# Kernel optimization log

Hardware: AMD Instinct MI355X
Metric: run time of the kernel (lower is better)

Reference implementation:

```python
import jax, jax.numpy as jnp
import numpy as np

_DIMS = [15, 30, 60, 90, 120, 90, 60, 30, 15, 10, 5, 1]


def setup_inputs() -> dict:
    key = jax.random.key(0)
    keys = jax.random.split(key, 1 + 2 * 11)
    inp = {"x": jax.random.normal(keys[0], (524288, 15), dtype=jnp.float32)}
    for i in range(11):
        fan_in, fan_out = _DIMS[i], _DIMS[i + 1]
        bound = 1.0 / np.sqrt(fan_in)
        inp[f"W{i+1}"] = jax.random.uniform(keys[1 + 2 * i], (fan_out, fan_in), minval=-bound, maxval=bound, dtype=jnp.float32)
        inp[f"b{i+1}"] = jax.random.uniform(keys[2 + 2 * i], (fan_out,), minval=-bound, maxval=bound, dtype=jnp.float32)
    return inp


def reference(x, W1, b1, W2, b2, W3, b3, W4, b4, W5, b5, W6, b6, W7, b7, W8, b8, W9, b9, W10, b10, W11, b11):
    Ws = [W1, W2, W3, W4, W5, W6, W7, W8, W9, W10, W11]
    bs = [b1, b2, b3, b4, b5, b6, b7, b8, b9, b10, b11]
    h = x
    # 10 Linear+ReLU layers, funnel 15->30->60->90->120->90->60->30->15->10->5
    for W, b in zip(Ws[:-1], bs[:-1]):
        h = jax.nn.relu(h @ W.T + b)
    # final Linear 5->1 + sigmoid
    return jax.nn.sigmoid(h @ Ws[-1].T + bs[-1])
```

## Files before the change

### kernel.cpp

```cpp
#include <hip/hip_runtime.h>
#include <math.h>


using bf16x8 = __attribute__((ext_vector_type(8))) short;
using f32x4  = __attribute__((ext_vector_type(4))) float;
using u16x8  = __attribute__((ext_vector_type(8))) unsigned short;
using u32x2  = __attribute__((ext_vector_type(2))) unsigned;
using u32x4  = __attribute__((ext_vector_type(4))) unsigned;
typedef __bf16 bf16x2_t __attribute__((ext_vector_type(2)));

namespace {
constexpr int NL = 11;
constexpr int IN_[NL]   = {15, 30, 60, 90, 120, 90, 60, 30, 15, 10, 5};
constexpr int OUT_[NL]  = {30, 60, 90, 120, 90, 60, 30, 15, 10, 5, 1};
constexpr int KP_[NL]   = {32, 32, 64, 96, 128, 96, 64, 32, 32, 32, 32};
constexpr int NP_[NL]   = {32, 64, 96, 128, 96, 64, 32, 16, 16, 16, 16};
constexpr int WOFF_[NL] = {0, 1024, 3072, 9216, 21504, 33792, 39936, 41984, 42496, 43008, 43520};
constexpr int WTOT      = 44032;
constexpr int WAVES     = 8;
constexpr int ROWS_PER_BLOCK = 512;
constexpr int ARENA     = 4096;
constexpr int LDS_BYTES = (WTOT + WAVES * ARENA) * 2;
}

__device__ __forceinline__ unsigned short f2bf(float f) {
    unsigned u = __float_as_uint(f);
    u += 0x7fffu + ((u >> 16) & 1u);
    return (unsigned short)(u >> 16);
}

__device__ __forceinline__ unsigned pk2(float a, float b) {
#if __has_builtin(__builtin_amdgcn_cvt_pk_bf16_f32)
    return __builtin_bit_cast(unsigned, __builtin_amdgcn_cvt_pk_bf16_f32(a, b));
#else
    bf16x2_t c;
    c[0] = (__bf16)a;
    c[1] = (__bf16)b;
    return __builtin_bit_cast(unsigned, c);
#endif
}

__device__ __forceinline__ u32x2 packrelu(f32x4 a) {
    u32x2 p;
    p[0] = pk2(fmaxf(a[0], 0.f), fmaxf(a[1], 0.f));
    p[1] = pk2(fmaxf(a[2], 0.f), fmaxf(a[3], 0.f));
    return p;
}

__device__ __forceinline__ bf16x8 xform(u32x2 pa, u32x2 pb, bool sel, int sA, int sB) {
    int a0 = __shfl((int)pa[0], sA);
    int b0 = __shfl((int)pb[0], sA);
    int a1 = __shfl((int)pa[1], sA);
    int b1 = __shfl((int)pb[1], sA);
    int a2 = __shfl((int)pa[0], sB);
    int b2 = __shfl((int)pb[0], sB);
    int a3 = __shfl((int)pa[1], sB);
    int b3 = __shfl((int)pb[1], sB);
    u32x4 r;
    r[0] = (unsigned)(sel ? b0 : a0);
    r[1] = (unsigned)(sel ? b1 : a1);
    r[2] = (unsigned)(sel ? b2 : a2);
    r[3] = (unsigned)(sel ? b3 : a3);
    return __builtin_bit_cast(bf16x8, r);
}

template <int L>
__device__ __forceinline__ void stage_w(const float* __restrict__ W,
                                        const float* __restrict__ B,
                                        short* wlds, int tid) {
    constexpr int KP = KP_[L], NP = NP_[L], INl = IN_[L], OUTl = OUT_[L];
    constexpr int NKT = KP / 32;
    for (int idx = tid; idx < NP * KP; idx += 512) {
        const int f    = idx >> 9;
        const int t    = idx & 511;
        const int quad = t >> 7;
        const int colc = (t >> 3) & 15;
        const int j    = t & 7;
        const int mt   = f / NKT;
        const int kt   = f - mt * NKT;
        const int m    = mt * 16 + colc;
        const int k    = kt * 32 + quad * 8 + j;
        float v = 0.f;
        if (m < OUTl) {
            if (k < INl) v = W[m * INl + k];
            else if (k == INl) v = B[m];
            else if (k == INl + 1) {
                float hf = __builtin_bit_cast(float, (unsigned)f2bf(B[m]) << 16);
                v = B[m] - hf;
            }
        } else if (m == OUTl || m == OUTl + 1) {
            if (k == INl) v = 1.f;
        }
        wlds[WOFF_[L] + idx] = (short)f2bf(v);
    }
}

template <int L>
__device__ __forceinline__ void layer_lds(const short* __restrict__ wlds,
                                          short* buf, int col, int quad, int fo) {
    constexpr int NKT  = KP_[L] / 32;
    constexpr int NMT  = NP_[L] / 16;
    constexpr int NKTN = KP_[L + 1] / 32;
    const short* wl = wlds + WOFF_[L];
    bf16x8 bin[4][NKT];
#pragma unroll
    for (int t = 0; t < 4; ++t)
#pragma unroll
        for (int kt = 0; kt < NKT; ++kt)
            bin[t][kt] = *(const bf16x8*)(buf + (t * NKT + kt) * 512 + fo);
    f32x4 acc[NMT][4];
#pragma unroll
    for (int mt = 0; mt < NMT; ++mt)
#pragma unroll
        for (int t = 0; t < 4; ++t)
            acc[mt][t] = f32x4{0.f, 0.f, 0.f, 0.f};
#pragma unroll
    for (int kt = 0; kt < NKT; ++kt)
#pragma unroll
        for (int mt = 0; mt < NMT; ++mt) {
            bf16x8 af = *(const bf16x8*)(wl + (mt * NKT + kt) * 512 + fo);
#pragma unroll
            for (int t = 0; t < 4; ++t)
                acc[mt][t] = __builtin_amdgcn_mfma_f32_16x16x32_bf16(af, bin[t][kt], acc[mt][t], 0, 0, 0);
        }
#pragma unroll
    for (int mt = 0; mt < NMT; ++mt) {
        const int wbase = (mt >> 1) * 512 + ((mt & 1) * 2 + (quad >> 1)) * 128 + col * 8 + (quad & 1) * 4;
#pragma unroll
        for (int t = 0; t < 4; ++t)
            *(u32x2*)(buf + t * NKTN * 512 + wbase) = packrelu(acc[mt][t]);
    }
}

template <int L>
__device__ __forceinline__ void reg_pair(const short* __restrict__ wlds, int g,
                                         const bf16x8 (&bin)[KP_[L] / 32][4],
                                         bf16x8 (&bout)[4],
                                         bool sel, int sA, int sB, int fo) {
    constexpr int NKT = KP_[L] / 32;
    const short* wl = wlds + WOFF_[L];
    f32x4 acc0[4], acc1[4];
#pragma unroll
    for (int t = 0; t < 4; ++t) {
        acc0[t] = f32x4{0.f, 0.f, 0.f, 0.f};
        acc1[t] = f32x4{0.f, 0.f, 0.f, 0.f};
    }
#pragma unroll
    for (int kt = 0; kt < NKT; ++kt) {
        bf16x8 a0 = *(const bf16x8*)(wl + ((2 * g) * NKT + kt) * 512 + fo);
        bf16x8 a1 = *(const bf16x8*)(wl + ((2 * g + 1) * NKT + kt) * 512 + fo);
#pragma unroll
        for (int t = 0; t < 4; ++t) {
            acc0[t] = __builtin_amdgcn_mfma_f32_16x16x32_bf16(a0, bin[kt][t], acc0[t], 0, 0, 0);
            acc1[t] = __builtin_amdgcn_mfma_f32_16x16x32_bf16(a1, bin[kt][t], acc1[t], 0, 0, 0);
        }
    }
#pragma unroll
    for (int t = 0; t < 4; ++t)
        bout[t] = xform(packrelu(acc0[t]), packrelu(acc1[t]), sel, sA, sB);
}

__device__ __forceinline__ void l5_to_lds(const short* __restrict__ wlds,
                                          const bf16x8 (&h5)[3][4],
                                          short* buf, int col, int quad, int fo) {
    const short* wl = wlds + WOFF_[5];
    f32x4 acc[4][4];
#pragma unroll
    for (int mt = 0; mt < 4; ++mt)
#pragma unroll
        for (int t = 0; t < 4; ++t)
            acc[mt][t] = f32x4{0.f, 0.f, 0.f, 0.f};
#pragma unroll
    for (int kt = 0; kt < 3; ++kt)
#pragma unroll
        for (int mt = 0; mt < 4; ++mt) {
            bf16x8 af = *(const bf16x8*)(wl + (mt * 3 + kt) * 512 + fo);
#pragma unroll
            for (int t = 0; t < 4; ++t)
                acc[mt][t] = __builtin_amdgcn_mfma_f32_16x16x32_bf16(af, h5[kt][t], acc[mt][t], 0, 0, 0);
        }
#pragma unroll
    for (int mt = 0; mt < 4; ++mt) {
        const int wbase = (mt >> 1) * 512 + ((mt & 1) * 2 + (quad >> 1)) * 128 + col * 8 + (quad & 1) * 4;
#pragma unroll
        for (int t = 0; t < 4; ++t)
            *(u32x2*)(buf + t * 2 * 512 + wbase) = packrelu(acc[mt][t]);
    }
}

__device__ __forceinline__ void layer_one4(bf16x8 af, short* buf, int col, int quad, int fo) {
    bf16x8 b[4];
#pragma unroll
    for (int t = 0; t < 4; ++t) b[t] = *(const bf16x8*)(buf + t * 512 + fo);
    f32x4 a[4];
#pragma unroll
    for (int t = 0; t < 4; ++t) {
        a[t] = f32x4{0.f, 0.f, 0.f, 0.f};
        a[t] = __builtin_amdgcn_mfma_f32_16x16x32_bf16(af, b[t], a[t], 0, 0, 0);
    }
    const int wbase = (quad >> 1) * 128 + col * 8 + (quad & 1) * 4;
#pragma unroll
    for (int t = 0; t < 4; ++t)
        *(u32x2*)(buf + t * 512 + wbase) = packrelu(a[t]);
    u16x8 z = {0, 0, 0, 0, 0, 0, 0, 0};
    if (!(quad & 1)) z[0] = (unsigned short)0x3F80;
    *(u16x8*)(buf + (quad >> 1) * 512 + (2 + (quad & 1)) * 128 + col * 8) = z;
    *(u16x8*)(buf + ((quad >> 1) + 2) * 512 + (2 + (quad & 1)) * 128 + col * 8) = z;
}

__device__ __forceinline__ float4 ld4(const float* p) {
    float4 t;
    __builtin_memcpy(&t, p, 16);
    return t;
}

__device__ __forceinline__ void fetch_x4(const float* __restrict__ x, int row0,
                                         int col, int quad, float4 (&xv)[4]) {
#pragma unroll
    for (int t = 0; t < 4; ++t) {
        const float* xr = x + (long)(row0 + t * 16 + col) * 15;
        if (quad < 3) {
            xv[t] = ld4(xr + quad * 4);
        } else {
            float4 u = ld4(xr + 11);
            xv[t] = make_float4(u.y, u.z, u.w, 1.f);
        }
    }
}

__device__ __forceinline__ void stage_x4(short* buf, const float4 (&xv)[4],
                                         int col, int quad) {
    const int off = (quad >> 1) * 128 + col * 8 + (quad & 1) * 4;
#pragma unroll
    for (int t = 0; t < 4; ++t) {
        u32x2 o;
        o[0] = pk2(xv[t].x, xv[t].y);
        o[1] = pk2(xv[t].z, xv[t].w);
        *(u32x2*)(buf + t * 512 + off) = o;
    }
    u16x8 z = {0, 0, 0, 0, 0, 0, 0, 0};
    if (!(quad & 1)) z[0] = (unsigned short)0x3F80;
    *(u16x8*)(buf + (quad >> 1) * 512 + (2 + (quad & 1)) * 128 + col * 8) = z;
    *(u16x8*)(buf + ((quad >> 1) + 2) * 512 + (2 + (quad & 1)) * 128 + col * 8) = z;
}

extern "C" __global__ void __launch_bounds__(512, 2)
mlp_fused(const float* __restrict__ x,
          const float* __restrict__ W0,  const float* __restrict__ B0,
          const float* __restrict__ W1,  const float* __restrict__ B1,
          const float* __restrict__ W2,  const float* __restrict__ B2,
          const float* __restrict__ W3,  const float* __restrict__ B3,
          const float* __restrict__ W4,  const float* __restrict__ B4,
          const float* __restrict__ W5,  const float* __restrict__ B5,
          const float* __restrict__ W6,  const float* __restrict__ B6,
          const float* __restrict__ W7,  const float* __restrict__ B7,
          const float* __restrict__ W8,  const float* __restrict__ B8,
          const float* __restrict__ W9,  const float* __restrict__ B9,
          const float* __restrict__ W10, const float* __restrict__ B10,
          float* __restrict__ out, int nchunks) {
    extern __shared__ __align__(16) short smem[];
    short* wlds = smem;
    short* act  = smem + WTOT;

    const int tid = threadIdx.x;

    stage_w<0>(W0, B0, wlds, tid);
    stage_w<1>(W1, B1, wlds, tid);
    stage_w<2>(W2, B2, wlds, tid);
    stage_w<3>(W3, B3, wlds, tid);
    stage_w<4>(W4, B4, wlds, tid);
    stage_w<5>(W5, B5, wlds, tid);
    stage_w<6>(W6, B6, wlds, tid);
    stage_w<7>(W7, B7, wlds, tid);
    stage_w<8>(W8, B8, wlds, tid);
    stage_w<9>(W9, B9, wlds, tid);
    stage_w<10>(W10, B10, wlds, tid);
    __syncthreads();

    const int wave = tid >> 6;
    const int lane = tid & 63;
    const int col  = lane & 15;
    const int quad = lane >> 4;
    short* buf = act + wave * ARENA;
    const int fo = quad * 128 + col * 8;
    const bool sel = quad >= 2;
    const int sA = col + 16 * (2 * (quad & 1));
    const int sB = sA + 16;

    const bf16x8 w7  = *(const bf16x8*)(wlds + WOFF_[7]  + fo);
    const bf16x8 w8  = *(const bf16x8*)(wlds + WOFF_[8]  + fo);
    const bf16x8 w9  = *(const bf16x8*)(wlds + WOFF_[9]  + fo);
    const bf16x8 w10 = *(const bf16x8*)(wlds + WOFF_[10] + fo);

    int chunk = blockIdx.x;
    float4 xv[4];
    if (chunk < nchunks)
        fetch_x4(x, chunk * ROWS_PER_BLOCK + wave * 64, col, quad, xv);

    for (; chunk < nchunks; chunk += gridDim.x) {
        const int row0 = chunk * ROWS_PER_BLOCK + wave * 64;
        stage_x4(buf, xv, col, quad);

        const int nxt = chunk + gridDim.x;
        if (nxt < nchunks)
            fetch_x4(x, nxt * ROWS_PER_BLOCK + wave * 64, col, quad, xv);

        layer_lds<0>(wlds, buf, col, quad, fo);
        layer_lds<1>(wlds, buf, col, quad, fo);

        bf16x8 h2[2][4];
#pragma unroll
        for (int kt = 0; kt < 2; ++kt)
#pragma unroll
            for (int t = 0; t < 4; ++t)
                h2[kt][t] = *(const bf16x8*)(buf + (t * 2 + kt) * 512 + fo);

        bf16x8 h3[3][4];
#pragma unroll
        for (int g = 0; g < 3; ++g)
            reg_pair<2>(wlds, g, h2, h3[g], sel, sA, sB, fo);

        bf16x8 h4[4][4];
#pragma unroll
        for (int g = 0; g < 4; ++g)
            reg_pair<3>(wlds, g, h3, h4[g], sel, sA, sB, fo);

        bf16x8 h5[3][4];
#pragma unroll
        for (int g = 0; g < 3; ++g)
            reg_pair<4>(wlds, g, h4, h5[g], sel, sA, sB, fo);

        l5_to_lds(wlds, h5, buf, col, quad, fo);

        layer_lds<6>(wlds, buf, col, quad, fo);
        layer_one4(w7, buf, col, quad, fo);
        layer_one4(w8, buf, col, quad, fo);
        layer_one4(w9, buf, col, quad, fo);

        {
            f32x4 a[4];
#pragma unroll
            for (int t = 0; t < 4; ++t) {
                bf16x8 b = *(const bf16x8*)(buf + t * 512 + fo);
                a[t] = f32x4{0.f, 0.f, 0.f, 0.f};
                a[t] = __builtin_amdgcn_mfma_f32_16x16x32_bf16(w10, b, a[t], 0, 0, 0);
            }
            if (quad == 0) {
#pragma unroll
                for (int t = 0; t < 4; ++t)
                    out[row0 + t * 16 + col] = 1.f / (1.f + __expf(-a[t][0]));
            }
        }
    }
}

extern "C" void kernel_launch(void* const* d_in, const int* in_sizes, int n_in,
                              void* d_out, int out_size, void* d_ws, size_t ws_size,
                              hipStream_t stream) {
    (void)n_in; (void)d_ws; (void)ws_size; (void)out_size;
    const float* x = (const float*)d_in[0];
    const float* W[11];
    const float* B[11];
    for (int i = 0; i < 11; ++i) {
        W[i] = (const float*)d_in[1 + 2 * i];
        B[i] = (const float*)d_in[2 + 2 * i];
    }
    const int nrows   = in_sizes[0] / 15;
    const int nchunks = nrows / ROWS_PER_BLOCK;

    hipFuncSetAttribute((const void*)mlp_fused,
                        hipFuncAttributeMaxDynamicSharedMemorySize, LDS_BYTES);

    mlp_fused<<<dim3(256), dim3(512), LDS_BYTES, stream>>>(
        x,
        W[0], B[0], W[1], B[1], W[2], B[2], W[3], B[3], W[4], B[4],
        W[5], B[5], W[6], B[6], W[7], B[7], W[8], B[8], W[9], B[9],
        W[10], B[10],
        (float*)d_out, nchunks);
}
```

Measured before the change: 201.9 us.

## Pipeline MLP layers across waves with register-resident weights and LDS handoff

Result: slower. 212.6 us (+5.3%).

```diff
diff --git a/kernel.cpp b/kernel.cpp
--- a/kernel.cpp
+++ b/kernel.cpp
@@ -11,16 +11,19 @@
 
 namespace {
 constexpr int NL = 11;
-constexpr int IN_[NL]   = {15, 30, 60, 90, 120, 90, 60, 30, 15, 10, 5};
-constexpr int OUT_[NL]  = {30, 60, 90, 120, 90, 60, 30, 15, 10, 5, 1};
-constexpr int KP_[NL]   = {32, 32, 64, 96, 128, 96, 64, 32, 32, 32, 32};
-constexpr int NP_[NL]   = {32, 64, 96, 128, 96, 64, 32, 16, 16, 16, 16};
-constexpr int WOFF_[NL] = {0, 1024, 3072, 9216, 21504, 33792, 39936, 41984, 42496, 43008, 43520};
-constexpr int WTOT      = 44032;
-constexpr int WAVES     = 8;
-constexpr int ROWS_PER_BLOCK = 512;
-constexpr int ARENA     = 4096;
-constexpr int LDS_BYTES = (WTOT + WAVES * ARENA) * 2;
+constexpr int IN_[NL]  = {15, 30, 60, 90, 120, 90, 60, 30, 15, 10, 5};
+constexpr int OUT_[NL] = {30, 60, 90, 120, 90, 60, 30, 15, 10, 5, 1};
+constexpr int KP_[NL]  = {32, 32, 64, 96, 128, 96, 64, 32, 32, 32, 32};
+constexpr int NP_[NL]  = {32, 64, 96, 128, 96, 64, 32, 16, 16, 16, 16};
+constexpr int E0 = 0;
+constexpr int E1 = 1024;
+constexpr int E2 = 5120;
+constexpr int E3 = 11264;
+constexpr int E4 = 19456;
+constexpr int E5 = 25600;
+constexpr int LDS_SHORTS = 29696;
+constexpr int LDS_BYTES  = LDS_SHORTS * 2;
+constexpr int G = 32;
 }
 
 __device__ __forceinline__ unsigned short f2bf(float f) {
@@ -64,10 +67,26 @@
     return __builtin_bit_cast(bf16x8, r);
 }
 
+__device__ __forceinline__ bf16x8 xform16(u32x2 p, int quad, int sA16, int sB16) {
+    int d0 = __shfl((int)p[0], sA16);
+    int d1 = __shfl((int)p[1], sA16);
+    int d2 = __shfl((int)p[0], sB16);
+    int d3 = __shfl((int)p[1], sB16);
+    u32x4 r;
+    if (quad < 2) {
+        r[0] = (unsigned)d0; r[1] = (unsigned)d1;
+        r[2] = (unsigned)d2; r[3] = (unsigned)d3;
+    } else {
+        r[0] = (quad == 2) ? 0x00003F80u : 0u;
+        r[1] = 0u; r[2] = 0u; r[3] = 0u;
+    }
+    return __builtin_bit_cast(bf16x8, r);
+}
+
 template <int L>
 __device__ __forceinline__ void stage_w(const float* __restrict__ W,
                                         const float* __restrict__ B,
-                                        short* wlds, int tid) {
+                                        short* s, int tid) {
     constexpr int KP = KP_[L], NP = NP_[L], INl = IN_[L], OUTl = OUT_[L];
     constexpr int NKT = KP / 32;
     for (int idx = tid; idx < NP * KP; idx += 512) {
@@ -91,121 +110,15 @@
         } else if (m == OUTl || m == OUTl + 1) {
             if (k == INl) v = 1.f;
         }
-        wlds[WOFF_[L] + idx] = (short)f2bf(v);
-    }
-}
-
-template <int L>
-__device__ __forceinline__ void layer_lds(const short* __restrict__ wlds,
-                                          short* buf, int col, int quad, int fo) {
-    constexpr int NKT  = KP_[L] / 32;
-    constexpr int NMT  = NP_[L] / 16;
-    constexpr int NKTN = KP_[L + 1] / 32;
-    const short* wl = wlds + WOFF_[L];
-    bf16x8 bin[4][NKT];
-#pragma unroll
-    for (int t = 0; t < 4; ++t)
-#pragma unroll
-        for (int kt = 0; kt < NKT; ++kt)
-            bin[t][kt] = *(const bf16x8*)(buf + (t * NKT + kt) * 512 + fo);
-    f32x4 acc[NMT][4];
-#pragma unroll
-    for (int mt = 0; mt < NMT; ++mt)
-#pragma unroll
-        for (int t = 0; t < 4; ++t)
-            acc[mt][t] = f32x4{0.f, 0.f, 0.f, 0.f};
-#pragma unroll
-    for (int kt = 0; kt < NKT; ++kt)
-#pragma unroll
-        for (int mt = 0; mt < NMT; ++mt) {
-            bf16x8 af = *(const bf16x8*)(wl + (mt * NKT + kt) * 512 + fo);
-#pragma unroll
-            for (int t = 0; t < 4; ++t)
-                acc[mt][t] = __builtin_amdgcn_mfma_f32_16x16x32_bf16(af, bin[t][kt], acc[mt][t], 0, 0, 0);
-        }
-#pragma unroll
-    for (int mt = 0; mt < NMT; ++mt) {
-        const int wbase = (mt >> 1) * 512 + ((mt & 1) * 2 + (quad >> 1)) * 128 + col * 8 + (quad & 1) * 4;
-#pragma unroll
-        for (int t = 0; t < 4; ++t)
-            *(u32x2*)(buf + t * NKTN * 512 + wbase) = packrelu(acc[mt][t]);
-    }
-}
-
-template <int L>
-__device__ __forceinline__ void reg_pair(const short* __restrict__ wlds, int g,
-                                         const bf16x8 (&bin)[KP_[L] / 32][4],
-                                         bf16x8 (&bout)[4],
-                                         bool sel, int sA, int sB, int fo) {
-    constexpr int NKT = KP_[L] / 32;
-    const short* wl = wlds + WOFF_[L];
-    f32x4 acc0[4], acc1[4];
-#pragma unroll
-    for (int t = 0; t < 4; ++t) {
-        acc0[t] = f32x4{0.f, 0.f, 0.f, 0.f};
-        acc1[t] = f32x4{0.f, 0.f, 0.f, 0.f};
-    }
-#pragma unroll
-    for (int kt = 0; kt < NKT; ++kt) {
-        bf16x8 a0 = *(const bf16x8*)(wl + ((2 * g) * NKT + kt) * 512 + fo);
-        bf16x8 a1 = *(const bf16x8*)(wl + ((2 * g + 1) * NKT + kt) * 512 + fo);
-#pragma unroll
-        for (int t = 0; t < 4; ++t) {
-            acc0[t] = __builtin_amdgcn_mfma_f32_16x16x32_bf16(a0, bin[kt][t], acc0[t], 0, 0, 0);
-            acc1[t] = __builtin_amdgcn_mfma_f32_16x16x32_bf16(a1, bin[kt][t], acc1[t], 0, 0, 0);
-        }
-    }
-#pragma unroll
-    for (int t = 0; t < 4; ++t)
-        bout[t] = xform(packrelu(acc0[t]), packrelu(acc1[t]), sel, sA, sB);
-}
-
-__device__ __forceinline__ void l5_to_lds(const short* __restrict__ wlds,
-                                          const bf16x8 (&h5)[3][4],
-                                          short* buf, int col, int quad, int fo) {
-    const short* wl = wlds + WOFF_[5];
-    f32x4 acc[4][4];
-#pragma unroll
-    for (int mt = 0; mt < 4; ++mt)
-#pragma unroll
-        for (int t = 0; t < 4; ++t)
-            acc[mt][t] = f32x4{0.f, 0.f, 0.f, 0.f};
-#pragma unroll
-    for (int kt = 0; kt < 3; ++kt)
-#pragma unroll
-        for (int mt = 0; mt < 4; ++mt) {
-            bf16x8 af = *(const bf16x8*)(wl + (mt * 3 + kt) * 512 + fo);
-#pragma unroll
-            for (int t = 0; t < 4; ++t)
-                acc[mt][t] = __builtin_amdgcn_mfma_f32_16x16x32_bf16(af, h5[kt][t], acc[mt][t], 0, 0, 0);
-        }
-#pragma unroll
-    for (int mt = 0; mt < 4; ++mt) {
-        const int wbase = (mt >> 1) * 512 + ((mt & 1) * 2 + (quad >> 1)) * 128 + col * 8 + (quad & 1) * 4;
-#pragma unroll
-        for (int t = 0; t < 4; ++t)
-            *(u32x2*)(buf + t * 2 * 512 + wbase) = packrelu(acc[mt][t]);
-    }
-}
-
-__device__ __forceinline__ void layer_one4(bf16x8 af, short* buf, int col, int quad, int fo) {
-    bf16x8 b[4];
-#pragma unroll
-    for (int t = 0; t < 4; ++t) b[t] = *(const bf16x8*)(buf + t * 512 + fo);
-    f32x4 a[4];
-#pragma unroll
-    for (int t = 0; t < 4; ++t) {
-        a[t] = f32x4{0.f, 0.f, 0.f, 0.f};
-        a[t] = __builtin_amdgcn_mfma_f32_16x16x32_bf16(af, b[t], a[t], 0, 0, 0);
-    }
-    const int wbase = (quad >> 1) * 128 + col * 8 + (quad & 1) * 4;
-#pragma unroll
-    for (int t = 0; t < 4; ++t)
-        *(u32x2*)(buf + t * 512 + wbase) = packrelu(a[t]);
-    u16x8 z = {0, 0, 0, 0, 0, 0, 0, 0};
-    if (!(quad & 1)) z[0] = (unsigned short)0x3F80;
-    *(u16x8*)(buf + (quad >> 1) * 512 + (2 + (quad & 1)) * 128 + col * 8) = z;
-    *(u16x8*)(buf + ((quad >> 1) + 2) * 512 + (2 + (quad & 1)) * 128 + col * 8) = z;
+        s[idx] = (short)f2bf(v);
+    }
+}
+
+__device__ __forceinline__ bf16x8 ldfrag(const short* p) { return *(const bf16x8*)p; }
+
+__device__ __forceinline__ void edge_write(short* tile, int mt, int col, int quad, f32x4 a) {
+    const int wb = (mt >> 1) * 512 + ((mt & 1) * 2 + (quad >> 1)) * 128 + col * 8 + (quad & 1) * 4;
+    *(u32x2*)(tile + wb) = packrelu(a);
 }
 
 __device__ __forceinline__ float4 ld4(const float* p) {
@@ -214,10 +127,10 @@
     return t;
 }
 
-__device__ __forceinline__ void fetch_x4(const float* __restrict__ x, int row0,
-                                         int col, int quad, float4 (&xv)[4]) {
-#pragma unroll
-    for (int t = 0; t < 4; ++t) {
+__device__ __forceinline__ void fetch_x2(const float* __restrict__ x, int row0,
+                                         int col, int quad, float4 (&xv)[2]) {
+#pragma unroll
+    for (int t = 0; t < 2; ++t) {
         const float* xr = x + (long)(row0 + t * 16 + col) * 15;
         if (quad < 3) {
             xv[t] = ld4(xr + quad * 4);
@@ -228,129 +141,274 @@
     }
 }
 
-__device__ __forceinline__ void stage_x4(short* buf, const float4 (&xv)[4],
-                                         int col, int quad) {
-    const int off = (quad >> 1) * 128 + col * 8 + (quad & 1) * 4;
-#pragma unroll
-    for (int t = 0; t < 4; ++t) {
-        u32x2 o;
-        o[0] = pk2(xv[t].x, xv[t].y);
-        o[1] = pk2(xv[t].z, xv[t].w);
-        *(u32x2*)(buf + t * 512 + off) = o;
-    }
-    u16x8 z = {0, 0, 0, 0, 0, 0, 0, 0};
-    if (!(quad & 1)) z[0] = (unsigned short)0x3F80;
-    *(u16x8*)(buf + (quad >> 1) * 512 + (2 + (quad & 1)) * 128 + col * 8) = z;
-    *(u16x8*)(buf + ((quad >> 1) + 2) * 512 + (2 + (quad & 1)) * 128 + col * 8) = z;
-}
-
-extern "C" __global__ void __launch_bounds__(512, 2)
-mlp_fused(const float* __restrict__ x,
-          const float* __restrict__ W0,  const float* __restrict__ B0,
-          const float* __restrict__ W1,  const float* __restrict__ B1,
-          const float* __restrict__ W2,  const float* __restrict__ B2,
-          const float* __restrict__ W3,  const float* __restrict__ B3,
-          const float* __restrict__ W4,  const float* __restrict__ B4,
-          const float* __restrict__ W5,  const float* __restrict__ B5,
-          const float* __restrict__ W6,  const float* __restrict__ B6,
-          const float* __restrict__ W7,  const float* __restrict__ B7,
-          const float* __restrict__ W8,  const float* __restrict__ B8,
-          const float* __restrict__ W9,  const float* __restrict__ B9,
-          const float* __restrict__ W10, const float* __restrict__ B10,
-          float* __restrict__ out, int nchunks) {
+extern "C" __global__ void __launch_bounds__(512, 4)
+mlp_pipe(const float* __restrict__ x,
+         const float* __restrict__ W0,  const float* __restrict__ B0,
+         const float* __restrict__ W1,  const float* __restrict__ B1,
+         const float* __restrict__ W2,  const float* __restrict__ B2,
+         const float* __restrict__ W3,  const float* __restrict__ B3,
+         const float* __restrict__ W4,  const float* __restrict__ B4,
+         const float* __restrict__ W5,  const float* __restrict__ B5,
+         const float* __restrict__ W6,  const float* __restrict__ B6,
+         const float* __restrict__ W7,  const float* __restrict__ B7,
+         const float* __restrict__ W8,  const float* __restrict__ B8,
+         const float* __restrict__ W9,  const float* __restrict__ B9,
+         const float* __restrict__ W10, const float* __restrict__ B10,
+         float* __restrict__ out, int ng) {
     extern __shared__ __align__(16) short smem[];
-    short* wlds = smem;
-    short* act  = smem + WTOT;
-
-    const int tid = threadIdx.x;
-
-    stage_w<0>(W0, B0, wlds, tid);
-    stage_w<1>(W1, B1, wlds, tid);
-    stage_w<2>(W2, B2, wlds, tid);
-    stage_w<3>(W3, B3, wlds, tid);
-    stage_w<4>(W4, B4, wlds, tid);
-    stage_w<5>(W5, B5, wlds, tid);
-    stage_w<6>(W6, B6, wlds, tid);
-    stage_w<7>(W7, B7, wlds, tid);
-    stage_w<8>(W8, B8, wlds, tid);
-    stage_w<9>(W9, B9, wlds, tid);
-    stage_w<10>(W10, B10, wlds, tid);
-    __syncthreads();
-
+    const int tid  = threadIdx.x;
     const int wave = tid >> 6;
     const int lane = tid & 63;
     const int col  = lane & 15;
     const int quad = lane >> 4;
-    short* buf = act + wave * ARENA;
-    const int fo = quad * 128 + col * 8;
+    const int fo   = quad * 128 + col * 8;
     const bool sel = quad >= 2;
-    const int sA = col + 16 * (2 * (quad & 1));
-    const int sB = sA + 16;
-
-    const bf16x8 w7  = *(const bf16x8*)(wlds + WOFF_[7]  + fo);
-    const bf16x8 w8  = *(const bf16x8*)(wlds + WOFF_[8]  + fo);
-    const bf16x8 w9  = *(const bf16x8*)(wlds + WOFF_[9]  + fo);
-    const bf16x8 w10 = *(const bf16x8*)(wlds + WOFF_[10] + fo);
-
-    int chunk = blockIdx.x;
-    float4 xv[4];
-    if (chunk < nchunks)
-        fetch_x4(x, chunk * ROWS_PER_BLOCK + wave * 64, col, quad, xv);
-
-    for (; chunk < nchunks; chunk += gridDim.x) {
-        const int row0 = chunk * ROWS_PER_BLOCK + wave * 64;
-        stage_x4(buf, xv, col, quad);
-
-        const int nxt = chunk + gridDim.x;
-        if (nxt < nchunks)
-            fetch_x4(x, nxt * ROWS_PER_BLOCK + wave * 64, col, quad, xv);
-
-        layer_lds<0>(wlds, buf, col, quad, fo);
-        layer_lds<1>(wlds, buf, col, quad, fo);
-
-        bf16x8 h2[2][4];
-#pragma unroll
-        for (int kt = 0; kt < 2; ++kt)
-#pragma unroll
-            for (int t = 0; t < 4; ++t)
-                h2[kt][t] = *(const bf16x8*)(buf + (t * 2 + kt) * 512 + fo);
-
-        bf16x8 h3[3][4];
-#pragma unroll
-        for (int g = 0; g < 3; ++g)
-            reg_pair<2>(wlds, g, h2, h3[g], sel, sA, sB, fo);
-
-        bf16x8 h4[4][4];
-#pragma unroll
-        for (int g = 0; g < 4; ++g)
-            reg_pair<3>(wlds, g, h3, h4[g], sel, sA, sB, fo);
-
-        bf16x8 h5[3][4];
-#pragma unroll
-        for (int g = 0; g < 3; ++g)
-            reg_pair<4>(wlds, g, h4, h5[g], sel, sA, sB, fo);
-
-        l5_to_lds(wlds, h5, buf, col, quad, fo);
-
-        layer_lds<6>(wlds, buf, col, quad, fo);
-        layer_one4(w7, buf, col, quad, fo);
-        layer_one4(w8, buf, col, quad, fo);
-        layer_one4(w9, buf, col, quad, fo);
-
-        {
-            f32x4 a[4];
-#pragma unroll
-            for (int t = 0; t < 4; ++t) {
-                bf16x8 b = *(const bf16x8*)(buf + t * 512 + fo);
-                a[t] = f32x4{0.f, 0.f, 0.f, 0.f};
-                a[t] = __builtin_amdgcn_mfma_f32_16x16x32_bf16(w10, b, a[t], 0, 0, 0);
-            }
-            if (quad == 0) {
-#pragma unroll
-                for (int t = 0; t < 4; ++t)
-                    out[row0 + t * 16 + col] = 1.f / (1.f + __expf(-a[t][0]));
+    const int sA   = col + 16 * (2 * (quad & 1));
+    const int sB   = sA + 16;
+    const int sA16 = col + 32 * (quad & 1);
+    const int sB16 = sA16 + 16;
+
+    bf16x8 wreg[12];
+#pragma unroll
+    for (int f = 0; f < 12; ++f) wreg[f] = bf16x8{0,0,0,0,0,0,0,0};
+
+    stage_w<0>(W0, B0, smem, tid); __syncthreads();
+    if (wave == 0) { wreg[0] = ldfrag(smem + fo); wreg[1] = ldfrag(smem + 512 + fo); }
+    __syncthreads();
+    stage_w<1>(W1, B1, smem, tid); __syncthreads();
+    if (wave == 0) {
+#pragma unroll
+        for (int f = 0; f < 4; ++f) wreg[2 + f] = ldfrag(smem + f * 512 + fo);
+    }
+    __syncthreads();
+    stage_w<2>(W2, B2, smem, tid); __syncthreads();
+    if (wave == 1) {
+#pragma unroll
+        for (int f = 0; f < 12; ++f) wreg[f] = ldfrag(smem + f * 512 + fo);
+    }
+    __syncthreads();
+    stage_w<3>(W3, B3, smem, tid); __syncthreads();
+    if (wave == 2) {
+#pragma unroll
+        for (int f = 0; f < 12; ++f) wreg[f] = ldfrag(smem + f * 512 + fo);
+    }
+    if (wave == 3) {
+#pragma unroll
+        for (int f = 0; f < 12; ++f) wreg[f] = ldfrag(smem + (12 + f) * 512 + fo);
+    }
+    __syncthreads();
+    stage_w<4>(W4, B4, smem, tid); __syncthreads();
+    if (wave == 4) {
+#pragma unroll
+        for (int f = 0; f < 12; ++f) wreg[f] = ldfrag(smem + f * 512 + fo);
+    }
+    if (wave == 5) {
+#pragma unroll
+        for (int f = 0; f < 12; ++f) wreg[f] = ldfrag(smem + (12 + f) * 512 + fo);
+    }
+    __syncthreads();
+    stage_w<5>(W5, B5, smem, tid); __syncthreads();
+    if (wave == 6) {
+#pragma unroll
+        for (int f = 0; f < 12; ++f) wreg[f] = ldfrag(smem + f * 512 + fo);
+    }
+    __syncthreads();
+    stage_w<6>(W6, B6, smem, tid); __syncthreads();
+    if (wave == 7) {
+#pragma unroll
+        for (int f = 0; f < 4; ++f) wreg[f] = ldfrag(smem + f * 512 + fo);
+    }
+    __syncthreads();
+    stage_w<7>(W7, B7, smem, tid); __syncthreads();
+    if (wave == 7) wreg[4] = ldfrag(smem + fo);
+    __syncthreads();
+    stage_w<8>(W8, B8, smem, tid); __syncthreads();
+    if (wave == 7) wreg[5] = ldfrag(smem + fo);
+    __syncthreads();
+    stage_w<9>(W9, B9, smem, tid); __syncthreads();
+    if (wave == 7) wreg[6] = ldfrag(smem + fo);
+    __syncthreads();
+    stage_w<10>(W10, B10, smem, tid); __syncthreads();
+    if (wave == 7) wreg[7] = ldfrag(smem + fo);
+    __syncthreads();
+
+    const int gbase = blockIdx.x * ng;
+    float4 xv[2];
+    if (wave == 0 && ng > 0) fetch_x2(x, gbase * G, col, quad, xv);
+
+    for (int n = 0; n < ng + 5; ++n) {
+        if (wave == 0) {
+            const int g = n;
+            if (g < ng) {
+                short* sx = smem + E0;
+                const int off = (quad >> 1) * 128 + col * 8 + (quad & 1) * 4;
+#pragma unroll
+                for (int t = 0; t < 2; ++t) {
+                    u32x2 o;
+                    o[0] = pk2(xv[t].x, xv[t].y);
+                    o[1] = pk2(xv[t].z, xv[t].w);
+                    *(u32x2*)(sx + t * 512 + off) = o;
+                }
+                u16x8 z = {0, 0, 0, 0, 0, 0, 0, 0};
+                if (!(quad & 1)) z[0] = (unsigned short)0x3F80;
+                *(u16x8*)(sx + (quad >> 1) * 512 + (2 + (quad & 1)) * 128 + col * 8) = z;
+
+                if (g + 1 < ng) fetch_x2(x, (gbase + g + 1) * G, col, quad, xv);
+
+                short* e1p = smem + E1 + (g & 1) * 2048;
+#pragma unroll
+                for (int t = 0; t < 2; ++t) {
+                    bf16x8 xb = ldfrag(sx + t * 512 + fo);
+                    f32x4 a0 = {0.f, 0.f, 0.f, 0.f}, a1 = {0.f, 0.f, 0.f, 0.f};
+                    a0 = __builtin_amdgcn_mfma_f32_16x16x32_bf16(wreg[0], xb, a0, 0, 0, 0);
+                    a1 = __builtin_amdgcn_mfma_f32_16x16x32_bf16(wreg[1], xb, a1, 0, 0, 0);
+                    bf16x8 h1 = xform(packrelu(a0), packrelu(a1), sel, sA, sB);
+                    f32x4 c[4];
+#pragma unroll
+                    for (int mt = 0; mt < 4; ++mt) c[mt] = f32x4{0.f, 0.f, 0.f, 0.f};
+#pragma unroll
+                    for (int mt = 0; mt < 4; ++mt)
+                        c[mt] = __builtin_amdgcn_mfma_f32_16x16x32_bf16(wreg[2 + mt], h1, c[mt], 0, 0, 0);
+#pragma unroll
+                    for (int mt = 0; mt < 4; ++mt)
+                        edge_write(e1p + t * 1024, mt, col, quad, c[mt]);
+                }
+            }
+        } else if (wave == 1) {
+            const int g = n - 1;
+            if (g >= 0 && g < ng) {
+                const short* e1p = smem + E1 + (g & 1) * 2048;
+                short* e2p = smem + E2 + (g & 1) * 3072;
+#pragma unroll
+                for (int t = 0; t < 2; ++t) {
+                    bf16x8 b0 = ldfrag(e1p + t * 1024 + fo);
+                    bf16x8 b1 = ldfrag(e1p + t * 1024 + 512 + fo);
+                    f32x4 acc[6];
+#pragma unroll
+                    for (int mt = 0; mt < 6; ++mt) acc[mt] = f32x4{0.f, 0.f, 0.f, 0.f};
+#pragma unroll
+                    for (int mt = 0; mt < 6; ++mt)
+                        acc[mt] = __builtin_amdgcn_mfma_f32_16x16x32_bf16(wreg[mt * 2], b0, acc[mt], 0, 0, 0);
+#pragma unroll
+                    for (int mt = 0; mt < 6; ++mt)
+                        acc[mt] = __builtin_amdgcn_mfma_f32_16x16x32_bf16(wreg[mt * 2 + 1], b1, acc[mt], 0, 0, 0);
+#pragma unroll
+                    for (int mt = 0; mt < 6; ++mt)
+                        edge_write(e2p + t * 1536, mt, col, quad, acc[mt]);
+                }
+            }
+        } else if (wave == 2 || wave == 3) {
+            const int g = n - 2;
+            if (g >= 0 && g < ng) {
+                const short* e2p = smem + E2 + (g & 1) * 3072;
+                short* e3p = smem + E3 + (g & 1) * 4096;
+                const int mo = (wave == 3) ? 4 : 0;
+                f32x4 acc[4][2];
+#pragma unroll
+                for (int mt = 0; mt < 4; ++mt)
+#pragma unroll
+                    for (int t = 0; t < 2; ++t) acc[mt][t] = f32x4{0.f, 0.f, 0.f, 0.f};
+#pragma unroll
+                for (int kt = 0; kt < 3; ++kt) {
+                    bf16x8 q0 = ldfrag(e2p + kt * 512 + fo);
+                    bf16x8 q1 = ldfrag(e2p + 1536 + kt * 512 + fo);
+#pragma unroll
+                    for (int mt = 0; mt < 4; ++mt) {
+                        acc[mt][0] = __builtin_amdgcn_mfma_f32_16x16x32_bf16(wreg[mt * 3 + kt], q0, acc[mt][0], 0, 0, 0);
+                        acc[mt][1] = __builtin_amdgcn_mfma_f32_16x16x32_bf16(wreg[mt * 3 + kt], q1, acc[mt][1], 0, 0, 0);
+                    }
+                }
+#pragma unroll
+                for (int mt = 0; mt < 4; ++mt)
+#pragma unroll
+                    for (int t = 0; t < 2; ++t)
+                        edge_write(e3p + t * 2048, mo + mt, col, quad, acc[mt][t]);
+            }
+        } else if (wave == 4 || wave == 5) {
+            const int g = n - 3;
+            if (g >= 0 && g < ng) {
+                const short* e3p = smem + E3 + (g & 1) * 4096;
+                short* e4p = smem + E4 + (g & 1) * 3072;
+                const int mo = (wave == 5) ? 3 : 0;
+                f32x4 acc[3][2];
+#pragma unroll
+                for (int mt = 0; mt < 3; ++mt)
+#pragma unroll
+                    for (int t = 0; t < 2; ++t) acc[mt][t] = f32x4{0.f, 0.f, 0.f, 0.f};
+#pragma unroll
+                for (int kt = 0; kt < 4; ++kt) {
+                    bf16x8 q0 = ldfrag(e3p + kt * 512 + fo);
+                    bf16x8 q1 = ldfrag(e3p + 2048 + kt * 512 + fo);
+#pragma unroll
+                    for (int mt = 0; mt < 3; ++mt) {
+                        const int f = mt * 4 + kt + ((wave == 5) ? 12 - 12 : 0);
+                        acc[mt][0] = __builtin_amdgcn_mfma_f32_16x16x32_bf16(wreg[f], q0, acc[mt][0], 0, 0, 0);
+                        acc[mt][1] = __builtin_amdgcn_mfma_f32_16x16x32_bf16(wreg[f], q1, acc[mt][1], 0, 0, 0);
+                    }
+                }
+#pragma unroll
+                for (int mt = 0; mt < 3; ++mt)
+#pragma unroll
+                    for (int t = 0; t < 2; ++t)
+                        edge_write(e4p + t * 1536, mo + mt, col, quad, acc[mt][t]);
+            }
+        } else if (wave == 6) {
+            const int g = n - 4;
+            if (g >= 0 && g < ng) {
+                const short* e4p = smem + E4 + (g & 1) * 3072;
+                short* e5p = smem + E5 + (g & 1) * 2048;
+                f32x4 acc[4][2];
+#pragma unroll
+                for (int mt = 0; mt < 4; ++mt)
+#pragma unroll
+                    for (int t = 0; t < 2; ++t) acc[mt][t] = f32x4{0.f, 0.f, 0.f, 0.f};
+#pragma unroll
+                for (int kt = 0; kt < 3; ++kt) {
+                    bf16x8 q0 = ldfrag(e4p + kt * 512 + fo);
+                    bf16x8 q1 = ldfrag(e4p + 1536 + kt * 512 + fo);
+#pragma unroll
+                    for (int mt = 0; mt < 4; ++mt) {
+                        acc[mt][0] = __builtin_amdgcn_mfma_f32_16x16x32_bf16(wreg[mt * 3 + kt], q0, acc[mt][0], 0, 0, 0);
+                        acc[mt][1] = __builtin_amdgcn_mfma_f32_16x16x32_bf16(wreg[mt * 3 + kt], q1, acc[mt][1], 0, 0, 0);
+                    }
+                }
+#pragma unroll
+                for (int mt = 0; mt < 4; ++mt)
+#pragma unroll
+                    for (int t = 0; t < 2; ++t)
+                        edge_write(e5p + t * 1024, mt, col, quad, acc[mt][t]);
+            }
+        } else {
+            const int g = n - 5;
+            if (g >= 0 && g < ng) {
+                const short* e5p = smem + E5 + (g & 1) * 2048;
+#pragma unroll
+                for (int t = 0; t < 2; ++t) {
+                    bf16x8 b0 = ldfrag(e5p + t * 1024 + fo);
+                    bf16x8 b1 = ldfrag(e5p + t * 1024 + 512 + fo);
+                    f32x4 c0 = {0.f, 0.f, 0.f, 0.f}, c1 = {0.f, 0.f, 0.f, 0.f};
+                    c0 = __builtin_amdgcn_mfma_f32_16x16x32_bf16(wreg[0], b0, c0, 0, 0, 0);
+                    c0 = __builtin_amdgcn_mfma_f32_16x16x32_bf16(wreg[1], b1, c0, 0, 0, 0);
+                    c1 = __builtin_amdgcn_mfma_f32_16x16x32_bf16(wreg[2], b0, c1, 0, 0, 0);
+                    c1 = __builtin_amdgcn_mfma_f32_16x16x32_bf16(wreg[3], b1, c1, 0, 0, 0);
+                    bf16x8 h7 = xform(packrelu(c0), packrelu(c1), sel, sA, sB);
+                    f32x4 d = {0.f, 0.f, 0.f, 0.f};
+                    d = __builtin_amdgcn_mfma_f32_16x16x32_bf16(wreg[4], h7, d, 0, 0, 0);
+                    bf16x8 h8 = xform16(packrelu(d), quad, sA16, sB16);
+                    f32x4 e = {0.f, 0.f, 0.f, 0.f};
+                    e = __builtin_amdgcn_mfma_f32_16x16x32_bf16(wreg[5], h8, e, 0, 0, 0);
+                    bf16x8 h9 = xform16(packrelu(e), quad, sA16, sB16);
+                    f32x4 ff = {0.f, 0.f, 0.f, 0.f};
+                    ff = __builtin_amdgcn_mfma_f32_16x16x32_bf16(wreg[6], h9, ff, 0, 0, 0);
+                    bf16x8 h10 = xform16(packrelu(ff), quad, sA16, sB16);
+                    f32x4 o = {0.f, 0.f, 0.f, 0.f};
+                    o = __builtin_amdgcn_mfma_f32_16x16x32_bf16(wreg[7], h10, o, 0, 0, 0);
+                    if (quad == 0)
+                        out[(gbase + g) * G + t * 16 + col] = 1.f / (1.f + __expf(-o[0]));
+                }
             }
         }
+        __syncthreads();
     }
 }
 
@@ -365,16 +423,17 @@
         W[i] = (const float*)d_in[1 + 2 * i];
         B[i] = (const float*)d_in[2 + 2 * i];
     }
-    const int nrows   = in_sizes[0] / 15;
-    const int nchunks = nrows / ROWS_PER_BLOCK;
-
-    hipFuncSetAttribute((const void*)mlp_fused,
+    const int nrows  = in_sizes[0] / 15;
+    const int blocks = 512;
+    const int ng     = (nrows / G) / blocks;
+
+    hipFuncSetAttribute((const void*)mlp_pipe,
                         hipFuncAttributeMaxDynamicSharedMemorySize, LDS_BYTES);
 
-    mlp_fused<<<dim3(256), dim3(512), LDS_BYTES, stream>>>(
+    mlp_pipe<<<dim3(blocks), dim3(512), LDS_BYTES, stream>>>(
         x,
         W[0], B[0], W[1], B[1], W[2], B[2], W[3], B[3], W[4], B[4],
         W[5], B[5], W[6], B[6], W[7], B[7], W[8], B[8], W[9], B[9],
         W[10], B[10],
-        (float*)d_out, nchunks);
-}
+        (float*)d_out, ng);
+}
```
